# Optimization experiments

Measured on AMD Instinct MI355X. Metric: run time of the kernel, lower is better.

## Reference

```python
import jax, jax.numpy as jnp
import numpy as np

E, H, L = 512, 1024, 4
VS, VT = 32000, 32000
B, SS, TT = 64, 48, 48
PAD = 0


def _cell(x, h, c, Wih, Whh, bih, bhh):
    # torch.nn.LSTMCell math: gate order i, f, g, o
    g = x @ Wih.T + h @ Whh.T + bih + bhh
    i, f, gg, o = jnp.split(g, 4, axis=-1)
    c = jax.nn.sigmoid(f) * c + jax.nn.sigmoid(i) * jnp.tanh(gg)
    h = jax.nn.sigmoid(o) * jnp.tanh(c)
    return h, c


def setup_inputs() -> dict:
    key = jax.random.key(0)
    ks = jax.random.split(key, 14)
    s = 0.05
    d = {}
    d['src_tokens'] = jax.random.randint(ks[0], (SS, B), 0, VS, dtype=jnp.int32)
    d['tgt_tokens'] = jax.random.randint(ks[1], (TT, B), 0, VT, dtype=jnp.int32)
    d['src_emb'] = jax.random.normal(ks[2], (VS, E)) * s
    d['tgt_emb'] = jax.random.normal(ks[3], (VT, E)) * s
    d['enc_Wih0'] = jax.random.normal(ks[4], (4 * H, E)) * s
    d['enc_WihR'] = jax.random.normal(ks[5], (L - 1, 4 * H, H)) * s
    d['enc_Whh'] = jax.random.normal(ks[6], (L, 4 * H, H)) * s
    d['enc_bih'] = jnp.zeros((L, 4 * H))
    d['enc_bhh'] = jnp.zeros((L, 4 * H))
    d['dec_Wih0'] = jax.random.normal(ks[7], (4 * H, E + H)) * s
    d['dec_WihR'] = jax.random.normal(ks[8], (L - 1, 4 * H, H)) * s
    d['dec_Whh'] = jax.random.normal(ks[9], (L, 4 * H, H)) * s
    d['dec_bih'] = jnp.zeros((L, 4 * H))
    d['dec_bhh'] = jnp.zeros((L, 4 * H))
    d['att_vec_W'] = jax.random.normal(ks[10], (H, 2 * H)) * s
    d['readout_W'] = jax.random.normal(ks[11], (VT, H)) * s
    return d


def _forward(src_tokens, tgt_tokens, src_emb, tgt_emb, enc_Wih0, enc_WihR,
             enc_Whh, enc_bih, enc_bhh, dec_Wih0, dec_WihR, dec_Whh, dec_bih,
             dec_bhh, att_vec_W, readout_W):
    src_x = src_emb[src_tokens]                      # [SS, B, E]
    h0 = jnp.zeros((L, B, H), src_emb.dtype)
    c0 = jnp.zeros((L, B, H), src_emb.dtype)

    def enc_step(carry, x_t):
        h, c = carry
        inp = x_t
        hs, cs = [], []
        for l in range(L):
            Wih = enc_Wih0 if l == 0 else enc_WihR[l - 1]
            hn, cn = _cell(inp, h[l], c[l], Wih, enc_Whh[l], enc_bih[l], enc_bhh[l])
            hs.append(hn); cs.append(cn)
            inp = hn
        return (jnp.stack(hs), jnp.stack(cs)), inp

    (hT, cT), enc_out = jax.lax.scan(enc_step, (h0, c0), src_x)
    src_enc = enc_out.transpose(1, 0, 2)             # [B, SS, H]

    # decoder init: last encoder layer (h, c) copied to every decoder layer
    hd = jnp.tile(hT[-1][None], (L, 1, 1))
    cd = jnp.tile(cT[-1][None], (L, 1, 1))
    tgt_x = tgt_emb[tgt_tokens[:-1]]                 # [TT-1, B, E]
    att0 = jnp.zeros((B, H), src_emb.dtype)

    def dec_step(carry, y_t):
        h, c, att = carry
        inp = jnp.concatenate([y_t, att], axis=-1)   # input feeding
        hs, cs = [], []
        for l in range(L):
            Wih = dec_Wih0 if l == 0 else dec_WihR[l - 1]
            hn, cn = _cell(inp, h[l], c[l], Wih, dec_Whh[l], dec_bih[l], dec_bhh[l])
            hs.append(hn); cs.append(cn)
            inp = hn
        h_top = hs[-1]
        # global attention, 'dot' score (full-length seqs -> all-zero mask is a no-op)
        scores = jnp.einsum('bsh,bh->bs', src_enc, h_top)
        alpha = jax.nn.softmax(scores, axis=-1)
        ctx = jnp.einsum('bs,bsh->bh', alpha, src_enc)
        att_t = jnp.tanh(jnp.concatenate([h_top, ctx], axis=-1) @ att_vec_W.T)
        return (jnp.stack(hs), jnp.stack(cs), att_t), att_t

    _, att_ves = jax.lax.scan(dec_step, (hd, cd, att0), tgt_x)  # [TT-1, B, H]

    logp = jax.nn.log_softmax(att_ves @ readout_W.T, axis=-1)   # [TT-1, B, VT]
    gold = tgt_tokens[1:]
    gold_lp = jnp.take_along_axis(logp, gold[..., None], axis=-1)[..., 0]
    mask = (gold != PAD).astype(logp.dtype)
    return (gold_lp * mask).sum(axis=0)              # [B]


def reference(src_tokens, tgt_tokens, src_emb, tgt_emb, enc_Wih0, enc_WihR,
              enc_Whh, enc_bih, enc_bhh, dec_Wih0, dec_WihR, dec_Whh, dec_bih,
              dec_bhh, att_vec_W, readout_W):
    return _forward(src_tokens, tgt_tokens, src_emb, tgt_emb, enc_Wih0,
                    enc_WihR, enc_Whh, enc_bih, enc_bhh, dec_Wih0, dec_WihR,
                    dec_Whh, dec_bih, dec_bhh, att_vec_W, readout_W)
```

## Files before the change

### kernel.cpp

```cpp
#include <hip/hip_runtime.h>


typedef __attribute__((ext_vector_type(8))) short bf16x8;
typedef __attribute__((ext_vector_type(4))) float f32x4;

#define SMEM_G  49152
#define SMEM_A  65536

#define NMT_SYNC_LIGHT()                                   \
  do {                                                     \
    asm volatile("s_waitcnt lgkmcnt(0)" ::: "memory");     \
    __builtin_amdgcn_s_barrier();                          \
    __builtin_amdgcn_sched_barrier(0);                     \
  } while (0)

__device__ __forceinline__ float bf2f(ushort u) {
  union { uint i; float f; } v; v.i = ((uint)u) << 16; return v.f;
}
__device__ __forceinline__ ushort f2bf(float x) {
  union { float f; uint i; } v; v.f = x;
  uint r = (v.i + 0x7fffu + ((v.i >> 16) & 1u)) >> 16;
  return (ushort)r;
}
__device__ __forceinline__ uint pack2(float x, float y) {
  return (uint)f2bf(x) | ((uint)f2bf(y) << 16);
}
__device__ __forceinline__ float sigm(float x) {
  return __fdividef(1.f, 1.f + __expf(-x));
}
__device__ __forceinline__ float tanhf_fast(float x) {
  const float e = __expf(2.f * x);
  return 1.f - __fdividef(2.f, e + 1.f);
}

__device__ __forceinline__ void gemm_term(
    const ushort* __restrict__ A, int lda,
    const ushort* __restrict__ W, int ldw,
    int K, int m0, int n0,
    f32x4 acc[4], char* s)
{
  const int tid = threadIdx.x;
  const int lane = tid & 63;
  const int w = tid >> 6;
  const int r0 = tid >> 3;
  const int cge = (tid & 7) << 3;
  const int so0 = r0 * 128 + (((tid & 7) << 4) ^ ((r0 & 7) << 4));
  const ushort* Ar0 = A + (size_t)(m0 + r0) * lda + cge;
  const ushort* Ar1 = A + (size_t)(m0 + r0 + 32) * lda + cge;
  const ushort* Wr0 = W + (size_t)(n0 + r0) * ldw + cge;
  const ushort* Wr1 = W + (size_t)(n0 + r0 + 32) * ldw + cge;
  const int NT = K >> 6;

  uint4 a0s0, a1s0, b0s0, b1s0;
  uint4 a0s1, a1s1, b0s1, b1s1;
  uint4 a0s2, a1s2, b0s2, b1s2;

  a0s0 = *(const uint4*)(Ar0);       a1s0 = *(const uint4*)(Ar1);
  b0s0 = *(const uint4*)(Wr0);       b1s0 = *(const uint4*)(Wr1);
  a0s1 = *(const uint4*)(Ar0 + 64);  a1s1 = *(const uint4*)(Ar1 + 64);
  b0s1 = *(const uint4*)(Wr0 + 64);  b1s1 = *(const uint4*)(Wr1 + 64);
  a0s2 = *(const uint4*)(Ar0 + 128); a1s2 = *(const uint4*)(Ar1 + 128);
  b0s2 = *(const uint4*)(Wr0 + 128); b1s2 = *(const uint4*)(Wr1 + 128);
  {
    char* sl = s;
    *(uint4*)(sl + so0) = a0s0;         *(uint4*)(sl + 4096 + so0) = a1s0;
    *(uint4*)(sl + 8192 + so0) = b0s0;  *(uint4*)(sl + 12288 + so0) = b1s0;
    sl = s + 16384;
    *(uint4*)(sl + so0) = a0s1;         *(uint4*)(sl + 4096 + so0) = a1s1;
    *(uint4*)(sl + 8192 + so0) = b0s1;  *(uint4*)(sl + 12288 + so0) = b1s1;
  }
  if (3 < NT) {
    a0s0 = *(const uint4*)(Ar0 + 192); a1s0 = *(const uint4*)(Ar1 + 192);
    b0s0 = *(const uint4*)(Wr0 + 192); b1s0 = *(const uint4*)(Wr1 + 192);
  }
  if (4 < NT) {
    a0s1 = *(const uint4*)(Ar0 + 256); a1s1 = *(const uint4*)(Ar1 + 256);
    b0s1 = *(const uint4*)(Wr0 + 256); b1s1 = *(const uint4*)(Wr1 + 256);
  }

  const int axor = (lane & 7) << 4;
  const int arow = (w * 16 + (lane & 15)) * 128;
  const int brow = (lane & 15) * 128;
  const int kb0 = (lane >> 4) << 4;

#define NMT_ROUND(KR, CUR, ST)                                                \
  do {                                                                        \
    NMT_SYNC_LIGHT();                                                         \
    if ((KR) + 2 < NT) {                                                      \
      char* sl_ = s + (ST) * 16384;                                           \
      *(uint4*)(sl_ + so0) = a0s##ST;                                         \
      *(uint4*)(sl_ + 4096 + so0) = a1s##ST;                                  \
      *(uint4*)(sl_ + 8192 + so0) = b0s##ST;                                  \
      *(uint4*)(sl_ + 12288 + so0) = b1s##ST;                                 \
      if ((KR) + 5 < NT) {                                                    \
        const int off_ = ((KR) + 5) << 6;                                     \
        a0s##ST = *(const uint4*)(Ar0 + off_);                                \
        a1s##ST = *(const uint4*)(Ar1 + off_);                                \
        b0s##ST = *(const uint4*)(Wr0 + off_);                                \
        b1s##ST = *(const uint4*)(Wr1 + off_);                                \
      }                                                                       \
    }                                                                         \
    char* cur_ = s + (CUR) * 16384;                                           \
    _Pragma("unroll")                                                         \
    for (int ks = 0; ks < 2; ++ks) {                                          \
      const int kb = (ks << 6) + kb0;                                         \
      bf16x8 af = *(const bf16x8*)(cur_ + arow + (kb ^ axor));                \
      _Pragma("unroll")                                                       \
      for (int nf = 0; nf < 4; ++nf) {                                        \
        bf16x8 bfr = *(const bf16x8*)(cur_ + 8192 + nf * 2048 + brow +        \
                                      (kb ^ axor));                           \
        acc[nf] = __builtin_amdgcn_mfma_f32_16x16x32_bf16(af, bfr, acc[nf],   \
                                                          0, 0, 0);           \
      }                                                                       \
    }                                                                         \
  } while (0)

  for (int kb_ = 0; kb_ < NT; kb_ += 3) {
    NMT_ROUND(kb_ + 0, 0, 2);
    if (kb_ + 1 < NT) NMT_ROUND(kb_ + 1, 1, 0);
    if (kb_ + 2 < NT) NMT_ROUND(kb_ + 2, 2, 1);
  }
#undef NMT_ROUND
  __syncthreads();
}

__device__ __forceinline__ void att_loadf(
    const float* H0, const float* H1, const float* C0, const float* C1,
    int kt, float4* fh, float4* fc)
{
#pragma unroll
  for (int q = 0; q < 8; ++q) {
    const int rh = q >> 2, sub = (q >> 1) & 1, vq = q & 1;
    const float* hp_ = rh ? H1 : H0;
    const float* cp_ = rh ? C1 : C0;
    fh[q] = *reinterpret_cast<const float4*>(hp_ + kt + sub * 64 + vq * 4);
    fc[q] = *reinterpret_cast<const float4*>(cp_ + kt + sub * 64 + vq * 4);
  }
}

__device__ __forceinline__ void att_store(
    char* buf, int soX, const float4* fh, const float4* fc)
{
#pragma unroll
  for (int rh = 0; rh < 2; ++rh)
#pragma unroll
    for (int sub = 0; sub < 2; ++sub) {
      const int q0 = rh * 4 + sub * 2;
      const float4 u = fh[q0], v = fc[q0];
      const float4 u2 = fh[q0 + 1], v2 = fc[q0 + 1];
      uint4 o;
      o.x = pack2(tanhf_fast(u.x + v.x), tanhf_fast(u.y + v.y));
      o.y = pack2(tanhf_fast(u.z + v.z), tanhf_fast(u.w + v.w));
      o.z = pack2(tanhf_fast(u2.x + v2.x), tanhf_fast(u2.y + v2.y));
      o.w = pack2(tanhf_fast(u2.z + v2.z), tanhf_fast(u2.w + v2.w));
      *reinterpret_cast<uint4*>(buf + sub * 8192 + rh * 4096 + soX) = o;
    }
}

__device__ __forceinline__ void gemm_att(
    const float* __restrict__ H, const float* __restrict__ C2,
    const ushort* __restrict__ W, int ldw, int n0,
    f32x4 acc[4], char* s)
{
  char* sA0 = s;
  char* sB0 = s + 16384;
  char* sA1 = s + 32768;
  char* sB1 = s + 49152;
  const int tid = threadIdx.x;
  const int lane = tid & 63;
  const int w = tid >> 6;
  const int r0 = tid >> 3;
  const int cge = (tid & 7) << 3;
  const int soX = r0 * 128 + (((tid & 7) << 4) ^ ((r0 & 7) << 4));
  const ushort* Wr0 = W + (size_t)(n0 + r0) * ldw + cge;
  const ushort* Wr1 = W + (size_t)(n0 + r0 + 32) * ldw + cge;
  const float* H0 = H + r0 * 1024 + cge;
  const float* H1 = H + (r0 + 32) * 1024 + cge;
  const float* C0 = C2 + r0 * 1024 + cge;
  const float* C1 = C2 + (r0 + 32) * 1024 + cge;

  float4 fh[8], fc[8];
  uint4 b0, b1, b2, b3;
  att_loadf(H0, H1, C0, C1, 0, fh, fc);
  att_store(sA0, soX, fh, fc);
  b0 = *reinterpret_cast<const uint4*>(Wr0);
  b1 = *reinterpret_cast<const uint4*>(Wr1);
  b2 = *reinterpret_cast<const uint4*>(Wr0 + 64);
  b3 = *reinterpret_cast<const uint4*>(Wr1 + 64);
  *reinterpret_cast<uint4*>(sB0 + soX) = b0;
  *reinterpret_cast<uint4*>(sB0 + 4096 + soX) = b1;
  *reinterpret_cast<uint4*>(sB0 + 8192 + soX) = b2;
  *reinterpret_cast<uint4*>(sB0 + 12288 + soX) = b3;
  att_loadf(H0, H1, C0, C1, 128, fh, fc);
  b0 = *reinterpret_cast<const uint4*>(Wr0 + 128);
  b1 = *reinterpret_cast<const uint4*>(Wr1 + 128);
  b2 = *reinterpret_cast<const uint4*>(Wr0 + 192);
  b3 = *reinterpret_cast<const uint4*>(Wr1 + 192);

  const int axor = (lane & 7) << 4;
  const int arow = (w * 16 + (lane & 15)) * 128;
  const int brow = (lane & 15) * 128;
  const int kb0 = (lane >> 4) << 4;
  for (int kt = 0; kt < 1024; kt += 128) {
    char* cA = (kt & 128) ? sA1 : sA0;
    char* cB = (kt & 128) ? sB1 : sB0;
    char* nA = (kt & 128) ? sA0 : sA1;
    char* nB = (kt & 128) ? sB0 : sB1;
    NMT_SYNC_LIGHT();
    if (kt + 128 < 1024) {
      att_store(nA, soX, fh, fc);
      *reinterpret_cast<uint4*>(nB + soX) = b0;
      *reinterpret_cast<uint4*>(nB + 4096 + soX) = b1;
      *reinterpret_cast<uint4*>(nB + 8192 + soX) = b2;
      *reinterpret_cast<uint4*>(nB + 12288 + soX) = b3;
      if (kt + 256 < 1024) {
        att_loadf(H0, H1, C0, C1, kt + 256, fh, fc);
        b0 = *reinterpret_cast<const uint4*>(Wr0 + kt + 256);
        b1 = *reinterpret_cast<const uint4*>(Wr1 + kt + 256);
        b2 = *reinterpret_cast<const uint4*>(Wr0 + kt + 320);
        b3 = *reinterpret_cast<const uint4*>(Wr1 + kt + 320);
      }
    }
#pragma unroll
    for (int ks = 0; ks < 4; ++ks) {
      const int sb = (ks >> 1) * 8192;
      const int kb = ((ks & 1) << 6) + kb0;
      bf16x8 af = *reinterpret_cast<const bf16x8*>(cA + sb + arow + (kb ^ axor));
#pragma unroll
      for (int nf = 0; nf < 4; ++nf) {
        bf16x8 bfr = *reinterpret_cast<const bf16x8*>(
            cB + sb + nf * 2048 + brow + (kb ^ axor));
        acc[nf] = __builtin_amdgcn_mfma_f32_16x16x32_bf16(af, bfr, acc[nf], 0, 0, 0);
      }
    }
  }
  __syncthreads();
}

__device__ __forceinline__ void store_f32(
    float* __restrict__ out, int ldo, int m0, int n0, f32x4 acc[4])
{
  const int tid = threadIdx.x, lane = tid & 63, w = tid >> 6;
  const int rbase = w * 16 + ((lane >> 4) << 2);
  const int cb = lane & 15;
#pragma unroll
  for (int nf = 0; nf < 4; ++nf)
#pragma unroll
    for (int r = 0; r < 4; ++r)
      out[(size_t)(m0 + rbase + r) * ldo + n0 + nf * 16 + cb] = acc[nf][r];
}

__device__ __forceinline__ void cell_store(
    float* smemF, f32x4 acc[4],
    float* __restrict__ c, ushort* __restrict__ hout,
    ushort* __restrict__ senc_t, int j0)
{
  const int tid = threadIdx.x, lane = tid & 63, w = tid >> 6;
  const int rbase = w * 16 + ((lane >> 4) << 2);
  const int cb = lane & 15;
  __syncthreads();
#pragma unroll
  for (int nf = 0; nf < 4; ++nf)
#pragma unroll
    for (int r = 0; r < 4; ++r)
      smemF[(rbase + r) * 68 + nf * 16 + cb] = acc[nf][r];
  __syncthreads();
#pragma unroll
  for (int i = 0; i < 4; ++i) {
    const int id = tid + i * 256;
    const int b = id >> 4, u = id & 15;
    const float g0 = smemF[b * 68 + u * 4 + 0];
    const float g1 = smemF[b * 68 + u * 4 + 1];
    const float g2 = smemF[b * 68 + u * 4 + 2];
    const float g3 = smemF[b * 68 + u * 4 + 3];
    const int off = b * 1024 + j0 + u;
    const float cold = c[off];
    const float cn = sigm(g1) * cold + sigm(g0) * tanhf_fast(g2);
    const float hv = sigm(g3) * tanhf_fast(cn);
    c[off] = cn;
    const ushort hb = f2bf(hv);
    hout[off] = hb;
    if (senc_t) senc_t[(size_t)b * 49152 + j0 + u] = hb;
  }
}

__global__ __launch_bounds__(256) void nmt_init(
    float* c, ushort* henc, float* hbAll, float* ctxAll)
{
  const int idx = blockIdx.x * 256 + threadIdx.x;
  if (idx < 262144) c[idx] = 0.f;
  if (idx < 65536) {
    hbAll[idx] = 0.f;
    ctxAll[idx] = 0.f;
    henc[idx] = 0;
    henc[(size_t)1 * 49 * 65536 + idx] = 0;
    henc[(size_t)2 * 49 * 65536 + idx] = 0;
    henc[(size_t)3 * 49 * 65536 + idx] = 0;
  }
}

__global__ __launch_bounds__(256) void nmt_convperm(
    const float* __restrict__ in, ushort* __restrict__ out,
    int L, int Kin, int col0, int Kout)
{
  const size_t idx = (size_t)blockIdx.x * 256 + threadIdx.x;
  const size_t total = (size_t)L * 4096 * Kout;
  if (idx >= total) return;
  const int k = (int)(idx % Kout);
  const size_t rem = idx / Kout;
  const int rp = (int)(rem % 4096);
  const int l = (int)(rem / 4096);
  const int j = rp >> 2, g = rp & 3;
  out[idx] = f2bf(in[((size_t)l * 4096 + g * 1024 + j) * Kin + col0 + k]);
}

__global__ __launch_bounds__(256) void nmt_convplain(
    const float* __restrict__ in, ushort* __restrict__ out, size_t n)
{
  const size_t idx = (size_t)blockIdx.x * 256 + threadIdx.x;
  if (idx < n) out[idx] = f2bf(in[idx]);
}

__global__ __launch_bounds__(256) void nmt_bias(
    const float* __restrict__ bih, const float* __restrict__ bhh, float* __restrict__ bc)
{
  const int idx = blockIdx.x * 256 + threadIdx.x;
  if (idx >= 4 * 4096) return;
  const int rp = idx & 4095, l = idx >> 12;
  const int j = rp >> 2, g = rp & 3;
  bc[idx] = bih[l * 4096 + g * 1024 + j] + bhh[l * 4096 + g * 1024 + j];
}

__global__ __launch_bounds__(256) void nmt_gather(
    const int* __restrict__ tok, const float* __restrict__ emb,
    ushort* __restrict__ out, int rows)
{
  const size_t idx = (size_t)blockIdx.x * 256 + threadIdx.x;
  if (idx >= (size_t)rows * 512) return;
  const int k = (int)(idx & 511);
  const int r = (int)(idx >> 9);
  out[idx] = f2bf(emb[(size_t)tok[r] * 512 + k]);
}

__global__ __launch_bounds__(256) void nmt_pre(
    const ushort* __restrict__ A, const ushort* __restrict__ Wp,
    const float* __restrict__ bc0, float* __restrict__ out, int K)
{
  __shared__ __align__(16) char smem[SMEM_G];
  const int m0 = blockIdx.x * 64, n0 = blockIdx.y * 64;
  const int lane = threadIdx.x & 63;
  const int cb = lane & 15;
  f32x4 acc[4];
#pragma unroll
  for (int nf = 0; nf < 4; ++nf) {
    const float bv = bc0[n0 + nf * 16 + cb];
#pragma unroll
    for (int r = 0; r < 4; ++r) acc[nf][r] = bv;
  }
  gemm_term(A, K, Wp, K, K, m0, n0, acc, smem);
  store_f32(out, 4096, m0, n0, acc);
}

__global__ __launch_bounds__(256) void nmt_decinit(
    const ushort* __restrict__ henc, float* c, ushort* h)
{
  const int idx = blockIdx.x * 256 + threadIdx.x;
  if (idx >= 65536) return;
  const ushort hv = henc[((size_t)3 * 49 + 48) * 65536 + idx];
  const float cv = c[3 * 65536 + idx];
  c[idx] = cv; c[65536 + idx] = cv; c[2 * 65536 + idx] = cv;
  h[idx] = hv; h[65536 + idx] = hv; h[2 * 65536 + idx] = hv; h[3 * 65536 + idx] = hv;
}

__global__ __launch_bounds__(256) void nmt_sv(
    const ushort* __restrict__ senc, const ushort* __restrict__ attW,
    ushort* __restrict__ SV)
{
  __shared__ __align__(16) char smem[SMEM_G];
  const int b = blockIdx.x;
  const int n0 = blockIdx.y * 64;
  const int tid = threadIdx.x, lane = tid & 63, w = tid >> 6;
  const int rbase = w * 16 + ((lane >> 4) << 2), cb = lane & 15;
  f32x4 acc[4];
#pragma unroll
  for (int nf = 0; nf < 4; ++nf)
#pragma unroll
    for (int r = 0; r < 4; ++r) acc[nf][r] = 0.f;
  gemm_term(senc + (size_t)b * 49152, 1024, attW + 1024, 2048, 1024, 0, n0,
            acc, smem);
#pragma unroll
  for (int nf = 0; nf < 4; ++nf)
#pragma unroll
    for (int r = 0; r < 4; ++r) {
      const int row = rbase + r;
      if (row < 48)
        SV[(size_t)b * 49152 + row * 1024 + n0 + nf * 16 + cb] = f2bf(acc[nf][r]);
    }
}

__global__ __launch_bounds__(256) void nmt_enc_cell(
    int u, int lo, ushort* __restrict__ henc, ushort* __restrict__ srcenc,
    float* __restrict__ c,
    const ushort* __restrict__ WihR, const ushort* __restrict__ Whh,
    const float* __restrict__ X0, const float* __restrict__ bcE)
{
  __shared__ __align__(16) char smem[SMEM_G];
  const int l = lo + blockIdx.y;
  const int t = u - l;
  const int n0 = blockIdx.x * 64;
  const int tid = threadIdx.x, lane = tid & 63, w = tid >> 6;
  const int rbase = w * 16 + ((lane >> 4) << 2), cb = lane & 15;
  f32x4 acc[4];
  if (l == 0) {
#pragma unroll
    for (int nf = 0; nf < 4; ++nf)
#pragma unroll
      for (int r = 0; r < 4; ++r)
        acc[nf][r] = X0[(size_t)t * 262144 + (size_t)(rbase + r) * 4096 + n0 + nf * 16 + cb];
  } else {
#pragma unroll
    for (int nf = 0; nf < 4; ++nf) {
      const float bv = bcE[l * 4096 + n0 + nf * 16 + cb];
#pragma unroll
      for (int r = 0; r < 4; ++r) acc[nf][r] = bv;
    }
    gemm_term(henc + ((size_t)(l - 1) * 49 + t + 1) * 65536, 1024,
              WihR + (size_t)(l - 1) * 4194304, 1024, 1024, 0, n0, acc, smem);
  }
  gemm_term(henc + ((size_t)l * 49 + t) * 65536, 1024,
            Whh + (size_t)l * 4194304, 1024, 1024, 0, n0, acc, smem);
  cell_store((float*)smem, acc, c + l * 65536,
             henc + ((size_t)l * 49 + t + 1) * 65536,
             (l == 3) ? (srcenc + t * 1024) : (ushort*)nullptr, n0 >> 2);
}

__global__ __launch_bounds__(256) void nmt_dec_stage(
    int l, const ushort* __restrict__ hp, ushort* __restrict__ hn,
    float* __restrict__ c,
    const ushort* __restrict__ Whh, const ushort* __restrict__ WihR,
    const ushort* __restrict__ Wd0a,
    const float* __restrict__ hbprev, const float* __restrict__ ctxprev,
    const float* __restrict__ Y0t, const float* __restrict__ bcD,
    float* __restrict__ pbuf)
{
  __shared__ __align__(16) char smem[SMEM_A];
  const int n0 = blockIdx.x * 64;
  const int tid = threadIdx.x, lane = tid & 63, w = tid >> 6;
  const int rbase = w * 16 + ((lane >> 4) << 2), cb = lane & 15;
  f32x4 acc[4];
  if (blockIdx.y == 0) {
    if (l == 0) {
#pragma unroll
      for (int nf = 0; nf < 4; ++nf)
#pragma unroll
        for (int r = 0; r < 4; ++r) {
          const size_t o = (size_t)(rbase + r) * 4096 + n0 + nf * 16 + cb;
          acc[nf][r] = Y0t[o] + pbuf[o];
        }
      gemm_att(hbprev, ctxprev, Wd0a, 1024, n0, acc, smem);
    } else {
#pragma unroll
      for (int nf = 0; nf < 4; ++nf)
#pragma unroll
        for (int r = 0; r < 4; ++r)
          acc[nf][r] = pbuf[(size_t)l * 262144 + (size_t)(rbase + r) * 4096 + n0 + nf * 16 + cb];
      gemm_term(hn + (l - 1) * 65536, 1024, WihR + (size_t)(l - 1) * 4194304,
                1024, 1024, 0, n0, acc, smem);
    }
    cell_store((float*)smem, acc, c + l * 65536, hn + l * 65536,
               (ushort*)nullptr, n0 >> 2);
  } else {
    const int lp = (l + 1) & 3;
    if (lp == 0) {
#pragma unroll
      for (int nf = 0; nf < 4; ++nf)
#pragma unroll
        for (int r = 0; r < 4; ++r) acc[nf][r] = 0.f;
      gemm_term(hn, 1024, Whh, 1024, 1024, 0, n0, acc, smem);
    } else {
#pragma unroll
      for (int nf = 0; nf < 4; ++nf) {
        const float bv = bcD[lp * 4096 + n0 + nf * 16 + cb];
#pragma unroll
        for (int r = 0; r < 4; ++r) acc[nf][r] = bv;
      }
      gemm_term(hp + lp * 65536, 1024, Whh + (size_t)lp * 4194304,
                1024, 1024, 0, n0, acc, smem);
    }
    store_f32(pbuf + (size_t)lp * 262144, 4096, 0, n0, acc);
  }
}

__global__ __launch_bounds__(256) void nmt_partial0(
    const ushort* __restrict__ h0, const ushort* __restrict__ Whh0,
    float* __restrict__ pbuf)
{
  __shared__ __align__(16) char smem[SMEM_G];
  const int n0 = blockIdx.x * 64;
  f32x4 acc[4];
#pragma unroll
  for (int nf = 0; nf < 4; ++nf)
#pragma unroll
    for (int r = 0; r < 4; ++r) acc[nf][r] = 0.f;
  gemm_term(h0, 1024, Whh0, 1024, 1024, 0, n0, acc, smem);
  store_f32(pbuf, 4096, 0, n0, acc);
}

__global__ __launch_bounds__(256) void nmt_attnAB(
    const ushort* __restrict__ h3, const ushort* __restrict__ senc,
    const ushort* __restrict__ SV, const ushort* __restrict__ attW,
    float* __restrict__ ctx2, float* __restrict__ hb)
{
  __shared__ __align__(16) char smem[SMEM_G];
  const int bid = blockIdx.x;
  const int tid = threadIdx.x, lane = tid & 63, w = tid >> 6;
  if (bid < 64) {
    float* sc = (float*)smem;
    float* al = (float*)smem + 64;
    const int b = bid;
    const ushort* sb = senc + (size_t)b * 49152;
    const ushort* vb = SV + (size_t)b * 49152;
    float hreg[16];
#pragma unroll
    for (int q = 0; q < 16; ++q) hreg[q] = bf2f(h3[b * 1024 + lane * 16 + q]);
    for (int s = w; s < 48; s += 4) {
      const ushort* vr = sb + s * 1024 + lane * 16;
      float p = 0.f;
#pragma unroll
      for (int q = 0; q < 16; ++q) p += bf2f(vr[q]) * hreg[q];
      for (int d = 1; d < 64; d <<= 1) p += __shfl_xor(p, d);
      if (lane == 0) sc[s] = p;
    }
    __syncthreads();
    if (tid < 64) {
      const float v = (lane < 48) ? sc[lane] : -3.4e38f;
      float m = v;
      for (int d = 1; d < 64; d <<= 1) m = fmaxf(m, __shfl_xor(m, d));
      float e = (lane < 48) ? expf(v - m) : 0.f;
      float s = e;
      for (int d = 1; d < 64; d <<= 1) s += __shfl_xor(s, d);
      al[lane] = e / s;
    }
    __syncthreads();
    const int k0 = tid * 4;
    float a0 = 0, a1 = 0, a2 = 0, a3 = 0;
    for (int s = 0; s < 48; ++s) {
      const float als = al[s];
      const ushort* vr = vb + s * 1024 + k0;
      a0 += als * bf2f(vr[0]); a1 += als * bf2f(vr[1]);
      a2 += als * bf2f(vr[2]); a3 += als * bf2f(vr[3]);
    }
    ctx2[b * 1024 + k0 + 0] = a0; ctx2[b * 1024 + k0 + 1] = a1;
    ctx2[b * 1024 + k0 + 2] = a2; ctx2[b * 1024 + k0 + 3] = a3;
  } else {
    const int n0 = (bid - 64) * 64;
    f32x4 acc[4];
#pragma unroll
    for (int nf = 0; nf < 4; ++nf)
#pragma unroll
      for (int r = 0; r < 4; ++r) acc[nf][r] = 0.f;
    gemm_term(h3, 1024, attW, 2048, 1024, 0, n0, acc, smem);
    store_f32(hb, 1024, 0, n0, acc);
  }
}

__global__ __launch_bounds__(256) void nmt_attves_k(
    const float* __restrict__ hbAll, const float* __restrict__ ctxAll,
    ushort* __restrict__ attves)
{
  const int i = blockIdx.x * 1024 + threadIdx.x * 4;
#pragma unroll
  for (int k = 0; k < 4; ++k) {
    const int j = i + k;
    attves[j] = f2bf(tanhf_fast(hbAll[j + 65536] + ctxAll[j + 65536]));
  }
}

__global__ __launch_bounds__(256) void nmt_readout(
    const ushort* __restrict__ attves, const ushort* __restrict__ routW,
    const int* __restrict__ tgt, float* __restrict__ pmax,
    float* __restrict__ psum, float* __restrict__ goldl)
{
  __shared__ __align__(16) char smem[SMEM_G];
  const int m0 = blockIdx.x * 64, n0 = blockIdx.y * 64;
  const int tid = threadIdx.x, lane = tid & 63, w = tid >> 6;
  const int rbase = w * 16 + ((lane >> 4) << 2), cb = lane & 15;
  f32x4 acc[4];
#pragma unroll
  for (int nf = 0; nf < 4; ++nf)
#pragma unroll
    for (int r = 0; r < 4; ++r) acc[nf][r] = 0.f;
  gemm_term(attves, 1024, routW, 1024, 1024, m0, n0, acc, smem);
#pragma unroll
  for (int r = 0; r < 4; ++r) {
    float lm = fmaxf(fmaxf(acc[0][r], acc[1][r]), fmaxf(acc[2][r], acc[3][r]));
    for (int d = 1; d < 16; d <<= 1) lm = fmaxf(lm, __shfl_xor(lm, d));
    float ls = 0.f;
#pragma unroll
    for (int nf = 0; nf < 4; ++nf) ls += expf(acc[nf][r] - lm);
    for (int d = 1; d < 16; d <<= 1) ls += __shfl_xor(ls, d);
    const int grow = m0 + rbase + r;
    if (cb == 0) {
      pmax[(size_t)grow * 500 + blockIdx.y] = lm;
      psum[(size_t)grow * 500 + blockIdx.y] = ls;
    }
    const int t = grow >> 6, b = grow & 63;
    const int gold = tgt[(t + 1) * 64 + b];
#pragma unroll
    for (int nf = 0; nf < 4; ++nf)
      if (n0 + nf * 16 + cb == gold) goldl[grow] = acc[nf][r];
  }
}

__global__ __launch_bounds__(64) void nmt_combine(
    const float* __restrict__ pmax, const float* __restrict__ psum,
    const float* __restrict__ goldl, const int* __restrict__ tgt,
    float* __restrict__ lpm)
{
  const int row = blockIdx.x;
  const int lane = threadIdx.x;
  float m = -3.4e38f, s = 0.f;
  for (int i = lane; i < 500; i += 64) {
    const float pm = pmax[(size_t)row * 500 + i];
    const float ps = psum[(size_t)row * 500 + i];
    if (pm > m) { s = s * expf(m - pm) + ps; m = pm; }
    else        { s += ps * expf(pm - m); }
  }
  for (int d = 1; d < 64; d <<= 1) {
    const float om = __shfl_xor(m, d), os = __shfl_xor(s, d);
    if (om > m) { s = s * expf(m - om) + os; m = om; }
    else        { s += os * expf(om - m); }
  }
  if (lane == 0) {
    const int t = row >> 6, b = row & 63;
    const int gold = tgt[(t + 1) * 64 + b];
    const float lp = goldl[row] - m - logf(s);
    lpm[row] = (gold != 0) ? lp : 0.f;
  }
}

__global__ __launch_bounds__(64) void nmt_final(
    const float* __restrict__ lpm, float* __restrict__ out)
{
  const int b = threadIdx.x;
  float s = 0.f;
  for (int t = 0; t < 47; ++t) s += lpm[t * 64 + b];
  out[b] = s;
}

extern "C" void kernel_launch(void* const* d_in, const int* in_sizes, int n_in,
                              void* d_out, int out_size, void* d_ws, size_t ws_size,
                              hipStream_t stream)
{
  (void)in_sizes; (void)n_in; (void)out_size; (void)ws_size;
  const int*   src_tok  = (const int*)d_in[0];
  const int*   tgt_tok  = (const int*)d_in[1];
  const float* src_emb  = (const float*)d_in[2];
  const float* tgt_emb  = (const float*)d_in[3];
  const float* eWih0    = (const float*)d_in[4];
  const float* eWihR    = (const float*)d_in[5];
  const float* eWhh     = (const float*)d_in[6];
  const float* ebih     = (const float*)d_in[7];
  const float* ebhh     = (const float*)d_in[8];
  const float* dWih0    = (const float*)d_in[9];
  const float* dWihR    = (const float*)d_in[10];
  const float* dWhh     = (const float*)d_in[11];
  const float* dbih     = (const float*)d_in[12];
  const float* dbhh     = (const float*)d_in[13];
  const float* attW_f   = (const float*)d_in[14];
  const float* routW_f  = (const float*)d_in[15];

  char* p = (char*)d_ws;
  auto alloc = [&](size_t bytes) { void* r = (void*)p; p += (bytes + 255) & ~(size_t)255; return r; };
  ushort* eWih0p = (ushort*)alloc((size_t)4096 * 512 * 2);
  ushort* eWihRp = (ushort*)alloc((size_t)3 * 4096 * 1024 * 2);
  ushort* eWhhp  = (ushort*)alloc((size_t)4 * 4096 * 1024 * 2);
  ushort* dWih0y = (ushort*)alloc((size_t)4096 * 512 * 2);
  ushort* dWih0a = (ushort*)alloc((size_t)4096 * 1024 * 2);
  ushort* dWihRp = (ushort*)alloc((size_t)3 * 4096 * 1024 * 2);
  ushort* dWhhp  = (ushort*)alloc((size_t)4 * 4096 * 1024 * 2);
  ushort* attWb  = (ushort*)alloc((size_t)1024 * 2048 * 2);
  ushort* routWb = (ushort*)alloc((size_t)32000 * 1024 * 2);
  ushort* srcx   = (ushort*)alloc((size_t)3072 * 512 * 2);
  ushort* tgtx   = (ushort*)alloc((size_t)3008 * 512 * 2);
  ushort* henc   = (ushort*)alloc((size_t)4 * 49 * 65536 * 2);
  ushort* hA     = (ushort*)alloc((size_t)4 * 65536 * 2);
  ushort* hB     = (ushort*)alloc((size_t)4 * 65536 * 2);
  ushort* srcenc = (ushort*)alloc((size_t)64 * 49152 * 2);
  ushort* SVbuf  = (ushort*)alloc((size_t)64 * 49152 * 2);
  ushort* attves = (ushort*)alloc((size_t)3008 * 1024 * 2);
  float*  hbAll  = (float*)alloc((size_t)48 * 65536 * 4);
  float*  ctxAll = (float*)alloc((size_t)48 * 65536 * 4);
  float*  pbuf   = (float*)alloc((size_t)4 * 262144 * 4);
  float*  X0     = (float*)alloc((size_t)3072 * 4096 * 4);
  float*  Y0     = (float*)alloc((size_t)3008 * 4096 * 4);
  float*  bcE    = (float*)alloc((size_t)16384 * 4);
  float*  bcD    = (float*)alloc((size_t)16384 * 4);
  float*  cbuf   = (float*)alloc((size_t)4 * 65536 * 4);
  float*  pmaxb  = (float*)alloc((size_t)3008 * 500 * 4);
  float*  psumb  = (float*)alloc((size_t)3008 * 500 * 4);
  float*  goldl  = (float*)alloc((size_t)3008 * 4);
  float*  lpm    = (float*)alloc((size_t)3008 * 4);

  const dim3 B256(256);
  auto g1 = [](size_t n) { return dim3((unsigned)((n + 255) / 256)); };

  nmt_init<<<g1(262144), B256, 0, stream>>>(cbuf, henc, hbAll, ctxAll);

  nmt_convperm<<<g1((size_t)4096 * 512), B256, 0, stream>>>(eWih0, eWih0p, 1, 512, 0, 512);
  nmt_convperm<<<g1((size_t)3 * 4096 * 1024), B256, 0, stream>>>(eWihR, eWihRp, 3, 1024, 0, 1024);
  nmt_convperm<<<g1((size_t)4 * 4096 * 1024), B256, 0, stream>>>(eWhh, eWhhp, 4, 1024, 0, 1024);
  nmt_convperm<<<g1((size_t)4096 * 512), B256, 0, stream>>>(dWih0, dWih0y, 1, 1536, 0, 512);
  nmt_convperm<<<g1((size_t)4096 * 1024), B256, 0, stream>>>(dWih0, dWih0a, 1, 1536, 512, 1024);
  nmt_convperm<<<g1((size_t)3 * 4096 * 1024), B256, 0, stream>>>(dWihR, dWihRp, 3, 1024, 0, 1024);
  nmt_convperm<<<g1((size_t)4 * 4096 * 1024), B256, 0, stream>>>(dWhh, dWhhp, 4, 1024, 0, 1024);
  nmt_convplain<<<g1((size_t)1024 * 2048), B256, 0, stream>>>(attW_f, attWb, (size_t)1024 * 2048);
  nmt_convplain<<<g1((size_t)32000 * 1024), B256, 0, stream>>>(routW_f, routWb, (size_t)32000 * 1024);
  nmt_bias<<<g1(16384), B256, 0, stream>>>(ebih, ebhh, bcE);
  nmt_bias<<<g1(16384), B256, 0, stream>>>(dbih, dbhh, bcD);
  nmt_gather<<<g1((size_t)3072 * 512), B256, 0, stream>>>(src_tok, src_emb, srcx, 3072);
  nmt_gather<<<g1((size_t)3008 * 512), B256, 0, stream>>>(tgt_tok, tgt_emb, tgtx, 3008);

  nmt_pre<<<dim3(48, 64), B256, 0, stream>>>(srcx, eWih0p, bcE, X0, 512);
  nmt_pre<<<dim3(47, 64), B256, 0, stream>>>(tgtx, dWih0y, bcD, Y0, 512);

  for (int u = 0; u < 51; ++u) {
    const int lo = (u > 47) ? (u - 47) : 0;
    const int hi = (u < 3) ? u : 3;
    nmt_enc_cell<<<dim3(64, hi - lo + 1), B256, 0, stream>>>(
        u, lo, henc, srcenc, cbuf, eWihRp, eWhhp, X0, bcE);
  }
  nmt_decinit<<<g1(65536), B256, 0, stream>>>(henc, cbuf, hA);
  nmt_sv<<<dim3(64, 16), B256, 0, stream>>>(srcenc, attWb, SVbuf);
  nmt_partial0<<<dim3(64), B256, 0, stream>>>(hA, dWhhp, pbuf);

  for (int t = 0; t < 47; ++t) {
    ushort* hp = (t & 1) ? hB : hA;
    ushort* hn = (t & 1) ? hA : hB;
    for (int l = 0; l < 4; ++l) {
      nmt_dec_stage<<<dim3(64, 2), B256, 0, stream>>>(
          l, hp, hn, cbuf, dWhhp, dWihRp, dWih0a,
          hbAll + (size_t)t * 65536, ctxAll + (size_t)t * 65536,
          Y0 + (size_t)t * 262144, bcD, pbuf);
    }
    nmt_attnAB<<<dim3(80), B256, 0, stream>>>(
        hn + 3 * 65536, srcenc, SVbuf, attWb,
        ctxAll + (size_t)(t + 1) * 65536, hbAll + (size_t)(t + 1) * 65536);
  }
  nmt_attves_k<<<dim3(3008), B256, 0, stream>>>(hbAll, ctxAll, attves);

  nmt_readout<<<dim3(47, 500), B256, 0, stream>>>(attves, routWb, tgt_tok,
                                                  pmaxb, psumb, goldl);
  nmt_combine<<<dim3(3008), dim3(64), 0, stream>>>(pmaxb, psumb, goldl, tgt_tok, lpm);
  nmt_final<<<dim3(1), dim3(64), 0, stream>>>(lpm, (float*)d_out);
}
```

Baseline: 4.496 ms.

## Fuse per-timestep decoder stages and attention into one kernel with grid barriers

Replaces the four per-layer decoder launches plus the attention launch per timestep with a single 256-block kernel. Inside it, layers are sequenced with an atomic-counter grid barrier. The Whh partial products for all upper layers are computed up front by the extra blocks in parallel with layer 0, instead of being pipelined one layer ahead. This aims to cut launch overhead and idle gaps between dependent small kernels. The cost is spin-wait barriers that rely on all 256 blocks being co-resident, and extra blocks that sit idle in later phases.

```diff
diff --git a/kernel.cpp b/kernel.cpp
--- a/kernel.cpp
+++ b/kernel.cpp
@@ -31,6 +31,20 @@
 __device__ __forceinline__ float tanhf_fast(float x) {
   const float e = __expf(2.f * x);
   return 1.f - __fdividef(2.f, e + 1.f);
+}
+
+__device__ __forceinline__ void gsync(int* bar, int target) {
+  __syncthreads();
+  if (threadIdx.x == 0) {
+    __threadfence();
+    __hip_atomic_fetch_add(bar, 1, __ATOMIC_RELEASE, __HIP_MEMORY_SCOPE_AGENT);
+    while (__hip_atomic_load(bar, __ATOMIC_RELAXED, __HIP_MEMORY_SCOPE_AGENT)
+           < target) {
+      __builtin_amdgcn_s_sleep(8);
+    }
+    (void)__hip_atomic_load(bar, __ATOMIC_ACQUIRE, __HIP_MEMORY_SCOPE_AGENT);
+  }
+  __syncthreads();
 }
 
 __device__ __forceinline__ void gemm_term(
@@ -285,9 +299,10 @@
 }
 
 __global__ __launch_bounds__(256) void nmt_init(
-    float* c, ushort* henc, float* hbAll, float* ctxAll)
+    float* c, ushort* henc, float* hbAll, float* ctxAll, int* bar)
 {
   const int idx = blockIdx.x * 256 + threadIdx.x;
+  if (idx == 0) bar[0] = 0;
   if (idx < 262144) c[idx] = 0.f;
   if (idx < 65536) {
     hbAll[idx] = 0.f;
@@ -434,31 +449,53 @@
              (l == 3) ? (srcenc + t * 1024) : (ushort*)nullptr, n0 >> 2);
 }
 
-__global__ __launch_bounds__(256) void nmt_dec_stage(
-    int l, const ushort* __restrict__ hp, ushort* __restrict__ hn,
+__global__ __launch_bounds__(256, 1) void nmt_dec_step(
+    int t, const ushort* __restrict__ hp, ushort* __restrict__ hn,
     float* __restrict__ c,
     const ushort* __restrict__ Whh, const ushort* __restrict__ WihR,
-    const ushort* __restrict__ Wd0a,
+    const ushort* __restrict__ Wd0a, const ushort* __restrict__ attW,
+    const ushort* __restrict__ senc, const ushort* __restrict__ SV,
     const float* __restrict__ hbprev, const float* __restrict__ ctxprev,
+    float* __restrict__ hbnext, float* __restrict__ ctxnext,
     const float* __restrict__ Y0t, const float* __restrict__ bcD,
-    float* __restrict__ pbuf)
+    float* __restrict__ pbuf, int* __restrict__ bar)
 {
   __shared__ __align__(16) char smem[SMEM_A];
-  const int n0 = blockIdx.x * 64;
+  const int bid = blockIdx.x;
   const int tid = threadIdx.x, lane = tid & 63, w = tid >> 6;
   const int rbase = w * 16 + ((lane >> 4) << 2), cb = lane & 15;
+  const int base = t * 1024;
   f32x4 acc[4];
-  if (blockIdx.y == 0) {
-    if (l == 0) {
-#pragma unroll
-      for (int nf = 0; nf < 4; ++nf)
-#pragma unroll
-        for (int r = 0; r < 4; ++r) {
-          const size_t o = (size_t)(rbase + r) * 4096 + n0 + nf * 16 + cb;
-          acc[nf][r] = Y0t[o] + pbuf[o];
-        }
-      gemm_att(hbprev, ctxprev, Wd0a, 1024, n0, acc, smem);
-    } else {
+
+  if (bid < 64) {
+    const int n0 = bid * 64;
+#pragma unroll
+    for (int nf = 0; nf < 4; ++nf)
+#pragma unroll
+      for (int r = 0; r < 4; ++r) {
+        const size_t o = (size_t)(rbase + r) * 4096 + n0 + nf * 16 + cb;
+        acc[nf][r] = Y0t[o] + pbuf[o];
+      }
+    gemm_att(hbprev, ctxprev, Wd0a, 1024, n0, acc, smem);
+    cell_store((float*)smem, acc, c, hn, (ushort*)nullptr, n0 >> 2);
+  } else {
+    const int lp = bid >> 6;
+    const int n0 = (bid & 63) * 64;
+#pragma unroll
+    for (int nf = 0; nf < 4; ++nf) {
+      const float bv = bcD[lp * 4096 + n0 + nf * 16 + cb];
+#pragma unroll
+      for (int r = 0; r < 4; ++r) acc[nf][r] = bv;
+    }
+    gemm_term(hp + lp * 65536, 1024, Whh + (size_t)lp * 4194304,
+              1024, 1024, 0, n0, acc, smem);
+    store_f32(pbuf + (size_t)lp * 262144, 4096, 0, n0, acc);
+  }
+  gsync(bar, base + 256);
+
+  for (int l = 1; l < 4; ++l) {
+    if (bid < 64) {
+      const int n0 = bid * 64;
 #pragma unroll
       for (int nf = 0; nf < 4; ++nf)
 #pragma unroll
@@ -466,54 +503,21 @@
           acc[nf][r] = pbuf[(size_t)l * 262144 + (size_t)(rbase + r) * 4096 + n0 + nf * 16 + cb];
       gemm_term(hn + (l - 1) * 65536, 1024, WihR + (size_t)(l - 1) * 4194304,
                 1024, 1024, 0, n0, acc, smem);
-    }
-    cell_store((float*)smem, acc, c + l * 65536, hn + l * 65536,
-               (ushort*)nullptr, n0 >> 2);
-  } else {
-    const int lp = (l + 1) & 3;
-    if (lp == 0) {
+      cell_store((float*)smem, acc, c + l * 65536, hn + l * 65536,
+                 (ushort*)nullptr, n0 >> 2);
+    } else if (l == 1 && bid < 128) {
+      const int n0 = (bid - 64) * 64;
 #pragma unroll
       for (int nf = 0; nf < 4; ++nf)
 #pragma unroll
         for (int r = 0; r < 4; ++r) acc[nf][r] = 0.f;
       gemm_term(hn, 1024, Whh, 1024, 1024, 0, n0, acc, smem);
-    } else {
-#pragma unroll
-      for (int nf = 0; nf < 4; ++nf) {
-        const float bv = bcD[lp * 4096 + n0 + nf * 16 + cb];
-#pragma unroll
-        for (int r = 0; r < 4; ++r) acc[nf][r] = bv;
-      }
-      gemm_term(hp + lp * 65536, 1024, Whh + (size_t)lp * 4194304,
-                1024, 1024, 0, n0, acc, smem);
-    }
-    store_f32(pbuf + (size_t)lp * 262144, 4096, 0, n0, acc);
-  }
-}
-
-__global__ __launch_bounds__(256) void nmt_partial0(
-    const ushort* __restrict__ h0, const ushort* __restrict__ Whh0,
-    float* __restrict__ pbuf)
-{
-  __shared__ __align__(16) char smem[SMEM_G];
-  const int n0 = blockIdx.x * 64;
-  f32x4 acc[4];
-#pragma unroll
-  for (int nf = 0; nf < 4; ++nf)
-#pragma unroll
-    for (int r = 0; r < 4; ++r) acc[nf][r] = 0.f;
-  gemm_term(h0, 1024, Whh0, 1024, 1024, 0, n0, acc, smem);
-  store_f32(pbuf, 4096, 0, n0, acc);
-}
-
-__global__ __launch_bounds__(256) void nmt_attnAB(
-    const ushort* __restrict__ h3, const ushort* __restrict__ senc,
-    const ushort* __restrict__ SV, const ushort* __restrict__ attW,
-    float* __restrict__ ctx2, float* __restrict__ hb)
-{
-  __shared__ __align__(16) char smem[SMEM_G];
-  const int bid = blockIdx.x;
-  const int tid = threadIdx.x, lane = tid & 63, w = tid >> 6;
+      store_f32(pbuf, 4096, 0, n0, acc);
+    }
+    gsync(bar, base + (l + 1) * 256);
+  }
+
+  const ushort* h3 = hn + 3 * 65536;
   if (bid < 64) {
     float* sc = (float*)smem;
     float* al = (float*)smem + 64;
@@ -550,18 +554,32 @@
       a0 += als * bf2f(vr[0]); a1 += als * bf2f(vr[1]);
       a2 += als * bf2f(vr[2]); a3 += als * bf2f(vr[3]);
     }
-    ctx2[b * 1024 + k0 + 0] = a0; ctx2[b * 1024 + k0 + 1] = a1;
-    ctx2[b * 1024 + k0 + 2] = a2; ctx2[b * 1024 + k0 + 3] = a3;
-  } else {
+    ctxnext[b * 1024 + k0 + 0] = a0; ctxnext[b * 1024 + k0 + 1] = a1;
+    ctxnext[b * 1024 + k0 + 2] = a2; ctxnext[b * 1024 + k0 + 3] = a3;
+  } else if (bid < 80) {
     const int n0 = (bid - 64) * 64;
-    f32x4 acc[4];
 #pragma unroll
     for (int nf = 0; nf < 4; ++nf)
 #pragma unroll
       for (int r = 0; r < 4; ++r) acc[nf][r] = 0.f;
     gemm_term(h3, 1024, attW, 2048, 1024, 0, n0, acc, smem);
-    store_f32(hb, 1024, 0, n0, acc);
-  }
+    store_f32(hbnext, 1024, 0, n0, acc);
+  }
+}
+
+__global__ __launch_bounds__(256) void nmt_partial0(
+    const ushort* __restrict__ h0, const ushort* __restrict__ Whh0,
+    float* __restrict__ pbuf)
+{
+  __shared__ __align__(16) char smem[SMEM_G];
+  const int n0 = blockIdx.x * 64;
+  f32x4 acc[4];
+#pragma unroll
+  for (int nf = 0; nf < 4; ++nf)
+#pragma unroll
+    for (int r = 0; r < 4; ++r) acc[nf][r] = 0.f;
+  gemm_term(h0, 1024, Whh0, 1024, 1024, 0, n0, acc, smem);
+  store_f32(pbuf, 4096, 0, n0, acc);
 }
 
 __global__ __launch_bounds__(256) void nmt_attves_k(
@@ -701,11 +719,12 @@
   float*  psumb  = (float*)alloc((size_t)3008 * 500 * 4);
   float*  goldl  = (float*)alloc((size_t)3008 * 4);
   float*  lpm    = (float*)alloc((size_t)3008 * 4);
+  int*    bar    = (int*)alloc(256);
 
   const dim3 B256(256);
   auto g1 = [](size_t n) { return dim3((unsigned)((n + 255) / 256)); };
 
-  nmt_init<<<g1(262144), B256, 0, stream>>>(cbuf, henc, hbAll, ctxAll);
+  nmt_init<<<g1(262144), B256, 0, stream>>>(cbuf, henc, hbAll, ctxAll, bar);
 
   nmt_convperm<<<g1((size_t)4096 * 512), B256, 0, stream>>>(eWih0, eWih0p, 1, 512, 0, 512);
   nmt_convperm<<<g1((size_t)3 * 4096 * 1024), B256, 0, stream>>>(eWihR, eWihRp, 3, 1024, 0, 1024);
@@ -737,15 +756,11 @@
   for (int t = 0; t < 47; ++t) {
     ushort* hp = (t & 1) ? hB : hA;
     ushort* hn = (t & 1) ? hA : hB;
-    for (int l = 0; l < 4; ++l) {
-      nmt_dec_stage<<<dim3(64, 2), B256, 0, stream>>>(
-          l, hp, hn, cbuf, dWhhp, dWihRp, dWih0a,
-          hbAll + (size_t)t * 65536, ctxAll + (size_t)t * 65536,
-          Y0 + (size_t)t * 262144, bcD, pbuf);
-    }
-    nmt_attnAB<<<dim3(80), B256, 0, stream>>>(
-        hn + 3 * 65536, srcenc, SVbuf, attWb,
-        ctxAll + (size_t)(t + 1) * 65536, hbAll + (size_t)(t + 1) * 65536);
+    nmt_dec_step<<<dim3(256), B256, 0, stream>>>(
+        t, hp, hn, cbuf, dWhhp, dWihRp, dWih0a, attWb, srcenc, SVbuf,
+        hbAll + (size_t)t * 65536, ctxAll + (size_t)t * 65536,
+        hbAll + (size_t)(t + 1) * 65536, ctxAll + (size_t)(t + 1) * 65536,
+        Y0 + (size_t)t * 262144, bcD, pbuf, bar);
   }
   nmt_attves_k<<<dim3(3008), B256, 0, stream>>>(hbAll, ctxAll, attves);
 
```

Measured after the change: 7.714 ms. 71.6% more time.

## Retile readout GEMM to 256x64 blocks with custom swizzled LDS MFMA loop

Applied to the files above, without the earlier changes.

Replaces the generic 64x64 gemm_term in the vocabulary readout with a dedicated kernel where each block computes four 64-row M tiles against one 64-column weight tile. Each loaded readout weight tile is reused across 256 rows, cutting repeated weight reads from global memory. The kernel uses XOR-swizzled shared memory and 16x16x32 bf16 MFMA. The attves buffer is padded to 3072 rows so the last partial group can read safely, and out-of-range tiles are skipped at writeback. Tradeoffs: the grid shrinks from 47x500 to 12x500 blocks, accumulator register pressure is higher, and the K loop has no software pipelining.

```diff
diff --git a/kernel.cpp b/kernel.cpp
--- a/kernel.cpp
+++ b/kernel.cpp
@@ -6,6 +6,7 @@
 
 #define SMEM_G  49152
 #define SMEM_A  65536
+#define SMEM_R  40960
 
 #define NMT_SYNC_LIGHT()                                   \
   do {                                                     \
@@ -581,34 +582,83 @@
     const int* __restrict__ tgt, float* __restrict__ pmax,
     float* __restrict__ psum, float* __restrict__ goldl)
 {
-  __shared__ __align__(16) char smem[SMEM_G];
-  const int m0 = blockIdx.x * 64, n0 = blockIdx.y * 64;
+  __shared__ __align__(16) char smem[SMEM_R];
+  const int g = blockIdx.x;
+  const int n0 = blockIdx.y * 64;
   const int tid = threadIdx.x, lane = tid & 63, w = tid >> 6;
   const int rbase = w * 16 + ((lane >> 4) << 2), cb = lane & 15;
-  f32x4 acc[4];
-#pragma unroll
-  for (int nf = 0; nf < 4; ++nf)
-#pragma unroll
-    for (int r = 0; r < 4; ++r) acc[nf][r] = 0.f;
-  gemm_term(attves, 1024, routW, 1024, 1024, m0, n0, acc, smem);
-#pragma unroll
-  for (int r = 0; r < 4; ++r) {
-    float lm = fmaxf(fmaxf(acc[0][r], acc[1][r]), fmaxf(acc[2][r], acc[3][r]));
-    for (int d = 1; d < 16; d <<= 1) lm = fmaxf(lm, __shfl_xor(lm, d));
-    float ls = 0.f;
-#pragma unroll
-    for (int nf = 0; nf < 4; ++nf) ls += expf(acc[nf][r] - lm);
-    for (int d = 1; d < 16; d <<= 1) ls += __shfl_xor(ls, d);
-    const int grow = m0 + rbase + r;
-    if (cb == 0) {
-      pmax[(size_t)grow * 500 + blockIdx.y] = lm;
-      psum[(size_t)grow * 500 + blockIdx.y] = ls;
-    }
-    const int t = grow >> 6, b = grow & 63;
-    const int gold = tgt[(t + 1) * 64 + b];
+  const int r0 = tid >> 3;
+  const int cge = (tid & 7) << 3;
+  const int soX = r0 * 128 + (((tid & 7) << 4) ^ ((r0 & 7) << 4));
+  const int axor = (lane & 7) << 4;
+  const int arow = (w * 16 + (lane & 15)) * 128;
+  const int brow = (lane & 15) * 128;
+  const int kb0 = (lane >> 4) << 4;
+
+  f32x4 acc[4][4];
+#pragma unroll
+  for (int mi = 0; mi < 4; ++mi)
 #pragma unroll
     for (int nf = 0; nf < 4; ++nf)
-      if (n0 + nf * 16 + cb == gold) goldl[grow] = acc[nf][r];
+#pragma unroll
+      for (int r = 0; r < 4; ++r) acc[mi][nf][r] = 0.f;
+
+  for (int kt = 0; kt < 1024; kt += 64) {
+    __syncthreads();
+#pragma unroll
+    for (int mi = 0; mi < 4; ++mi) {
+      const size_t mr = (size_t)(g * 256 + mi * 64 + r0) * 1024 + kt + cge;
+      *(uint4*)(smem + mi * 8192 + soX) = *(const uint4*)(attves + mr);
+      *(uint4*)(smem + mi * 8192 + 4096 + soX) = *(const uint4*)(attves + mr + 32 * 1024);
+    }
+    {
+      const size_t wr = (size_t)(n0 + r0) * 1024 + kt + cge;
+      *(uint4*)(smem + 32768 + soX) = *(const uint4*)(routW + wr);
+      *(uint4*)(smem + 32768 + 4096 + soX) = *(const uint4*)(routW + wr + 32 * 1024);
+    }
+    __syncthreads();
+#pragma unroll
+    for (int ks = 0; ks < 2; ++ks) {
+      const int kb = (ks << 6) + kb0;
+      bf16x8 bf0 = *(const bf16x8*)(smem + 32768 + 0 * 2048 + brow + (kb ^ axor));
+      bf16x8 bf1 = *(const bf16x8*)(smem + 32768 + 1 * 2048 + brow + (kb ^ axor));
+      bf16x8 bf2 = *(const bf16x8*)(smem + 32768 + 2 * 2048 + brow + (kb ^ axor));
+      bf16x8 bf3 = *(const bf16x8*)(smem + 32768 + 3 * 2048 + brow + (kb ^ axor));
+#pragma unroll
+      for (int mi = 0; mi < 4; ++mi) {
+        bf16x8 af = *(const bf16x8*)(smem + mi * 8192 + arow + (kb ^ axor));
+        acc[mi][0] = __builtin_amdgcn_mfma_f32_16x16x32_bf16(af, bf0, acc[mi][0], 0, 0, 0);
+        acc[mi][1] = __builtin_amdgcn_mfma_f32_16x16x32_bf16(af, bf1, acc[mi][1], 0, 0, 0);
+        acc[mi][2] = __builtin_amdgcn_mfma_f32_16x16x32_bf16(af, bf2, acc[mi][2], 0, 0, 0);
+        acc[mi][3] = __builtin_amdgcn_mfma_f32_16x16x32_bf16(af, bf3, acc[mi][3], 0, 0, 0);
+      }
+    }
+  }
+
+#pragma unroll
+  for (int mi = 0; mi < 4; ++mi) {
+    const int gm = g * 4 + mi;
+    if (gm >= 47) continue;
+#pragma unroll
+    for (int r = 0; r < 4; ++r) {
+      float lm = fmaxf(fmaxf(acc[mi][0][r], acc[mi][1][r]),
+                       fmaxf(acc[mi][2][r], acc[mi][3][r]));
+      for (int d = 1; d < 16; d <<= 1) lm = fmaxf(lm, __shfl_xor(lm, d));
+      float ls = 0.f;
+#pragma unroll
+      for (int nf = 0; nf < 4; ++nf) ls += expf(acc[mi][nf][r] - lm);
+      for (int d = 1; d < 16; d <<= 1) ls += __shfl_xor(ls, d);
+      const int grow = gm * 64 + rbase + r;
+      if (cb == 0) {
+        pmax[(size_t)grow * 500 + blockIdx.y] = lm;
+        psum[(size_t)grow * 500 + blockIdx.y] = ls;
+      }
+      const int t = grow >> 6, b = grow & 63;
+      const int gold = tgt[(t + 1) * 64 + b];
+#pragma unroll
+      for (int nf = 0; nf < 4; ++nf)
+        if (n0 + nf * 16 + cb == gold) goldl[grow] = acc[mi][nf][r];
+    }
   }
 }
 
@@ -688,7 +738,7 @@
   ushort* hB     = (ushort*)alloc((size_t)4 * 65536 * 2);
   ushort* srcenc = (ushort*)alloc((size_t)64 * 49152 * 2);
   ushort* SVbuf  = (ushort*)alloc((size_t)64 * 49152 * 2);
-  ushort* attves = (ushort*)alloc((size_t)3008 * 1024 * 2);
+  ushort* attves = (ushort*)alloc((size_t)3072 * 1024 * 2);
   float*  hbAll  = (float*)alloc((size_t)48 * 65536 * 4);
   float*  ctxAll = (float*)alloc((size_t)48 * 65536 * 4);
   float*  pbuf   = (float*)alloc((size_t)4 * 262144 * 4);
@@ -749,7 +799,7 @@
   }
   nmt_attves_k<<<dim3(3008), B256, 0, stream>>>(hbAll, ctxAll, attves);
 
-  nmt_readout<<<dim3(47, 500), B256, 0, stream>>>(attves, routWb, tgt_tok,
+  nmt_readout<<<dim3(12, 500), B256, 0, stream>>>(attves, routWb, tgt_tok,
                                                   pmaxb, psumb, goldl);
   nmt_combine<<<dim3(3008), dim3(64), 0, stream>>>(pmaxb, psumb, goldl, tgt_tok, lpm);
   nmt_final<<<dim3(1), dim3(64), 0, stream>>>(lpm, (float*)d_out);
```

Result: no change. 4.498 ms (+0.0%).
